# Optimization experiments

Measured on AMD Instinct MI355X. Metric: run time of the kernel, lower is better.

Reference implementation:

```python
import jax, jax.numpy as jnp
import numpy as np

D_MODEL = 1024
D_HEAD = 128
B, S = 4, 4096


def apply_rope(x, cos, sin):
    # x: [B,S,d_head], cos/sin: [S, d_head//2]
    half = x.shape[-1] // 2
    x1, x2 = x[..., :half], x[..., half:]
    cos = cos[None, :, :].astype(x.dtype)
    sin = sin[None, :, :].astype(x.dtype)
    return jnp.concatenate([x1 * cos - x2 * sin, x1 * sin + x2 * cos], axis=-1)


def setup_inputs() -> dict:
    key = jax.random.key(0)
    ks = jax.random.split(key, 10)
    x = jax.random.normal(ks[0], (B, S, D_MODEL), dtype=jnp.float32)
    # realistic RoPE tables
    half = D_HEAD // 2
    inv_freq = 1.0 / (10000.0 ** (np.arange(0, half, dtype=np.float32) / half))
    pos = np.arange(S, dtype=np.float32)
    ang = pos[:, None] * inv_freq[None, :]
    cos = jnp.asarray(np.cos(ang), dtype=jnp.float32)
    sin = jnp.asarray(np.sin(ang), dtype=jnp.float32)
    # True where key index > query index (masked positions)
    causal_mask = jnp.triu(jnp.ones((S, S), dtype=bool), k=1)
    scale_w = 1.0 / np.sqrt(D_MODEL)
    Wq1 = jax.random.normal(ks[1], (D_MODEL, D_HEAD), dtype=jnp.float32) * scale_w
    Wq2 = jax.random.normal(ks[2], (D_MODEL, D_HEAD), dtype=jnp.float32) * scale_w
    Wk1 = jax.random.normal(ks[3], (D_MODEL, D_HEAD), dtype=jnp.float32) * scale_w
    Wk2 = jax.random.normal(ks[4], (D_MODEL, D_HEAD), dtype=jnp.float32) * scale_w
    Wv = jax.random.normal(ks[5], (D_MODEL, D_HEAD), dtype=jnp.float32) * scale_w
    Wo = jax.random.normal(ks[6], (D_HEAD, D_MODEL), dtype=jnp.float32) * (1.0 / np.sqrt(D_HEAD))
    return {"x": x, "cos": cos, "sin": sin, "causal_mask": causal_mask,
            "Wq1": Wq1, "Wq2": Wq2, "Wk1": Wk1, "Wk2": Wk2, "Wv": Wv, "Wo": Wo}


def reference(x, cos, sin, causal_mask, Wq1, Wq2, Wk1, Wk2, Wv, Wo):
    q1 = apply_rope(jnp.einsum('bsD,Dd->bsd', x, Wq1), cos, sin)
    q2 = apply_rope(jnp.einsum('bsD,Dd->bsd', x, Wq2), cos, sin)
    k1 = apply_rope(jnp.einsum('bsD,Dd->bsd', x, Wk1), cos, sin)
    k2 = apply_rope(jnp.einsum('bsD,Dd->bsd', x, Wk2), cos, sin)
    v = jnp.einsum('bsD,Dd->bsd', x, Wv)
    scale = 1.0 / np.sqrt(D_HEAD)
    a1 = jnp.einsum('bsd,btd->bst', q1, k1) * scale
    a2 = jnp.einsum('bsd,btd->bst', q2, k2) * scale
    a = jnp.where(causal_mask[None, :, :], 0.0, a1 * a2)
    out = jnp.einsum('bst,btd->bsd', a, v)
    return jnp.einsum('bsd,dD->bsD', out, Wo)
```

## Files before the change

kernel.cpp:

```cpp
#include <hip/hip_runtime.h>
#include <stdint.h>
#include <stddef.h>

typedef _Float16 f16;
typedef __attribute__((ext_vector_type(8))) _Float16 f16x8;
typedef __attribute__((ext_vector_type(4))) _Float16 f16x4;
typedef __attribute__((ext_vector_type(16))) float f32x16;
typedef __attribute__((ext_vector_type(4))) float floatx4;

#define MFMA(a, b, c) __builtin_amdgcn_mfma_f32_32x32x16_f16((a), (b), (c), 0, 0, 0)

typedef const __attribute__((address_space(1))) void gvoid_t;
typedef __attribute__((address_space(3))) void svoid_t;

__device__ __forceinline__ void gload_lds16(const void* g, void* l) {
  __builtin_amdgcn_global_load_lds((gvoid_t*)g, (svoid_t*)l, 16, 0, 0);
}

__global__ __launch_bounds__(256) void k_cvt_f16(const float* __restrict__ in,
                                                 f16* __restrict__ out, int n4) {
  int i = blockIdx.x * 256 + threadIdx.x;
  if (i < n4) {
    floatx4 v = ((const floatx4*)in)[i];
    f16x4 o;
    o[0] = (f16)v[0]; o[1] = (f16)v[1]; o[2] = (f16)v[2]; o[3] = (f16)v[3];
    ((f16x4*)out)[i] = o;
  }
}

__global__ __launch_bounds__(256) void k_transpose_cvt(const float* __restrict__ W,
                                                       f16* __restrict__ Wt, int K, int N) {
  __shared__ float t[32][33];
  int k0 = blockIdx.x * 32, n0 = blockIdx.y * 32;
  int tx = threadIdx.x & 31, ty = threadIdx.x >> 5;
#pragma unroll
  for (int i = 0; i < 4; ++i)
    t[ty + 8 * i][tx] = W[(size_t)(k0 + ty + 8 * i) * N + n0 + tx];
  __syncthreads();
#pragma unroll
  for (int i = 0; i < 4; ++i)
    Wt[(size_t)(n0 + ty + 8 * i) * K + k0 + tx] = (f16)t[tx][ty + 8 * i];
}

__global__ __launch_bounds__(256, 2) void k_gemm(const f16* __restrict__ A,
                                                 const f16* __restrict__ Bt,
                                                 float* __restrict__ C,
                                                 int M, int N, int K) {
  __shared__ __align__(16) f16 As[128 * 64];
  __shared__ __align__(16) f16 Bs[128 * 64];
  int tid = threadIdx.x;
  int wave = tid >> 6, lane = tid & 63;
  int m0 = blockIdx.y * 128, n0 = blockIdx.x * 128;
  int wm = (wave >> 1) * 64, wn = (wave & 1) * 64;
  int rl = lane & 31, h = lane >> 5;
  int srow = lane >> 3, sslot = lane & 7;

  f32x16 acc[2][2];
#pragma unroll
  for (int mb = 0; mb < 2; ++mb)
#pragma unroll
    for (int nb = 0; nb < 2; ++nb)
#pragma unroll
      for (int r = 0; r < 16; ++r) acc[mb][nb][r] = 0.f;

  for (int k0 = 0; k0 < K; k0 += 64) {
    __syncthreads();
#pragma unroll
    for (int c = 0; c < 4; ++c) {
      int chunk = c * 4 + wave;
      int r = chunk * 8 + srow;
      int cb = sslot ^ (r & 7);
      gload_lds16(A + (size_t)(m0 + r) * K + k0 + cb * 8, As + chunk * 512);
      gload_lds16(Bt + (size_t)(n0 + r) * K + k0 + cb * 8, Bs + chunk * 512);
    }
    __syncthreads();

#pragma unroll
    for (int kb = 0; kb < 4; ++kb) {
      int s = 2 * kb + h;
      f16x8 af[2], bf[2];
#pragma unroll
      for (int mb = 0; mb < 2; ++mb) {
        int r = wm + mb * 32 + rl;
        af[mb] = *(const f16x8*)(As + r * 64 + (s ^ (r & 7)) * 8);
      }
#pragma unroll
      for (int nb = 0; nb < 2; ++nb) {
        int r = wn + nb * 32 + rl;
        bf[nb] = *(const f16x8*)(Bs + r * 64 + (s ^ (r & 7)) * 8);
      }
#pragma unroll
      for (int mb = 0; mb < 2; ++mb)
#pragma unroll
        for (int nb = 0; nb < 2; ++nb)
          acc[mb][nb] = MFMA(af[mb], bf[nb], acc[mb][nb]);
    }
  }

#pragma unroll
  for (int mb = 0; mb < 2; ++mb)
#pragma unroll
    for (int nb = 0; nb < 2; ++nb)
#pragma unroll
      for (int r = 0; r < 16; ++r) {
        int i = m0 + wm + mb * 32 + (r & 3) + 8 * (r >> 2) + 4 * h;
        int j = n0 + wn + nb * 32 + rl;
        C[(size_t)i * N + j] = acc[mb][nb][r];
      }
}

__global__ __launch_bounds__(256, 2) void k_proj(const f16* __restrict__ A,
                                                 const f16* __restrict__ Bt,
                                                 const float* __restrict__ cosp,
                                                 const float* __restrict__ sinp,
                                                 f16* __restrict__ q1h, f16* __restrict__ q2h,
                                                 f16* __restrict__ k1h, f16* __restrict__ k2h,
                                                 f16* __restrict__ vh) {
  __shared__ __align__(16) f16 As[128 * 64];
  __shared__ __align__(16) f16 Bs[128 * 64];
  int tid = threadIdx.x;
  int wave = tid >> 6, lane = tid & 63;
  int m0 = blockIdx.y * 128, n0 = blockIdx.x;
  int wm = wave * 32;
  int rl = lane & 31, h = lane >> 5;
  int srow = lane >> 3, sslot = lane & 7;
  const f16* Bmat = Bt + (size_t)n0 * 128 * 1024;

  f32x16 acc[4];
#pragma unroll
  for (int nb = 0; nb < 4; ++nb)
#pragma unroll
    for (int r = 0; r < 16; ++r) acc[nb][r] = 0.f;

  for (int k0 = 0; k0 < 1024; k0 += 64) {
    __syncthreads();
#pragma unroll
    for (int c = 0; c < 4; ++c) {
      int chunk = c * 4 + wave;
      int r = chunk * 8 + srow;
      int cb = sslot ^ (r & 7);
      gload_lds16(A + (size_t)(m0 + r) * 1024 + k0 + cb * 8, As + chunk * 512);
      gload_lds16(Bmat + (size_t)r * 1024 + k0 + cb * 8, Bs + chunk * 512);
    }
    __syncthreads();

#pragma unroll
    for (int kb = 0; kb < 4; ++kb) {
      int s = 2 * kb + h;
      int ra = wm + rl;
      f16x8 af = *(const f16x8*)(As + ra * 64 + (s ^ (ra & 7)) * 8);
      f16x8 bf[4];
#pragma unroll
      for (int nb = 0; nb < 4; ++nb) {
        int rb = nb * 32 + rl;
        bf[nb] = *(const f16x8*)(Bs + rb * 64 + (s ^ (rb & 7)) * 8);
      }
#pragma unroll
      for (int nb = 0; nb < 4; ++nb) acc[nb] = MFMA(af, bf[nb], acc[nb]);
    }
  }

  if (n0 == 4) {
#pragma unroll
    for (int r = 0; r < 16; ++r) {
      int irow = (r & 3) + 8 * (r >> 2) + 4 * h;
      int gr = m0 + wm + irow;
#pragma unroll
      for (int nb = 0; nb < 4; ++nb)
        vh[(size_t)gr * 128 + nb * 32 + rl] = (f16)acc[nb][r];
    }
  } else {
    f16* outp = (n0 == 0) ? q1h : (n0 == 1) ? q2h : (n0 == 2) ? k1h : k2h;
#pragma unroll
    for (int r = 0; r < 16; ++r) {
      int irow = (r & 3) + 8 * (r >> 2) + 4 * h;
      int gr = m0 + wm + irow;
      int s = gr & 4095;
#pragma unroll
      for (int nb = 0; nb < 2; ++nb) {
        int d = nb * 32 + rl;
        float c = cosp[s * 64 + d], sn = sinp[s * 64 + d];
        float a = acc[nb][r], bb = acc[nb + 2][r];
        outp[(size_t)gr * 128 + d]      = (f16)(a * c - bb * sn);
        outp[(size_t)gr * 128 + 64 + d] = (f16)(a * sn + bb * c);
      }
    }
  }
}

__global__ __launch_bounds__(256) void k_vtrans16(const f16* __restrict__ vh,
                                                  f16* __restrict__ vt) {
  __shared__ unsigned short t[32][33];
  int r0 = blockIdx.x * 32, d0 = blockIdx.y * 32;
  int tx = threadIdx.x & 31, ty = threadIdx.x >> 5;
#pragma unroll
  for (int i = 0; i < 4; ++i)
    t[ty + 8 * i][tx] = ((const unsigned short*)vh)[(size_t)(r0 + ty + 8 * i) * 128 + d0 + tx];
  __syncthreads();
  int b = r0 >> 12, s0 = r0 & 4095;
#pragma unroll
  for (int i = 0; i < 4; ++i)
    ((unsigned short*)vt)[((size_t)(b * 128 + d0 + ty + 8 * i)) * 4096 + s0 + tx] =
        t[tx][ty + 8 * i];
}

__global__ __launch_bounds__(256, 2) void k_s(const f16* __restrict__ q1h,
                                              const f16* __restrict__ q2h,
                                              const f16* __restrict__ k1h,
                                              const f16* __restrict__ k2h,
                                              f16* __restrict__ P) {
  __shared__ __align__(16) f16 A1[128 * 64];
  __shared__ __align__(16) f16 A2[128 * 64];
  __shared__ __align__(16) f16 B1[128 * 64];
  __shared__ __align__(16) f16 B2[128 * 64];
  int bid0 = blockIdx.x;
  int bid = (bid0 & 7) * 264 + (bid0 >> 3);
  int b = bid / 528, t = bid % 528;
  int i = (int)((sqrtf(8.f * t + 1.f) - 1.f) * 0.5f);
  if ((i + 1) * (i + 2) / 2 <= t) ++i;
  if (i * (i + 1) / 2 > t) --i;
  int j = t - i * (i + 1) / 2;

  int tid = threadIdx.x;
  int wave = tid >> 6, lane = tid & 63;
  int wm = (wave >> 1) * 64, wn = (wave & 1) * 64;
  int rl = lane & 31, h = lane >> 5;
  int srow = lane >> 3, sslot = lane & 7;
  size_t rowA = (size_t)b * 4096 + i * 128;
  size_t rowB = (size_t)b * 4096 + j * 128;

  f32x16 acc1[2][2], acc2[2][2];
#pragma unroll
  for (int mb = 0; mb < 2; ++mb)
#pragma unroll
    for (int nb = 0; nb < 2; ++nb)
#pragma unroll
      for (int r = 0; r < 16; ++r) { acc1[mb][nb][r] = 0.f; acc2[mb][nb][r] = 0.f; }

  for (int k0 = 0; k0 < 128; k0 += 64) {
    __syncthreads();
#pragma unroll
    for (int c = 0; c < 4; ++c) {
      int chunk = c * 4 + wave;
      int r = chunk * 8 + srow;
      int cb = sslot ^ (r & 7);
      gload_lds16(q1h + (rowA + r) * 128 + k0 + cb * 8, A1 + chunk * 512);
      gload_lds16(q2h + (rowA + r) * 128 + k0 + cb * 8, A2 + chunk * 512);
      gload_lds16(k1h + (rowB + r) * 128 + k0 + cb * 8, B1 + chunk * 512);
      gload_lds16(k2h + (rowB + r) * 128 + k0 + cb * 8, B2 + chunk * 512);
    }
    __syncthreads();

#pragma unroll
    for (int kb = 0; kb < 4; ++kb) {
      int s = 2 * kb + h;
      f16x8 a1f[2], a2f[2], b1f[2], b2f[2];
#pragma unroll
      for (int mb = 0; mb < 2; ++mb) {
        int r = wm + mb * 32 + rl;
        int off = r * 64 + (s ^ (r & 7)) * 8;
        a1f[mb] = *(const f16x8*)(A1 + off);
        a2f[mb] = *(const f16x8*)(A2 + off);
      }
#pragma unroll
      for (int nb = 0; nb < 2; ++nb) {
        int r = wn + nb * 32 + rl;
        int off = r * 64 + (s ^ (r & 7)) * 8;
        b1f[nb] = *(const f16x8*)(B1 + off);
        b2f[nb] = *(const f16x8*)(B2 + off);
      }
#pragma unroll
      for (int mb = 0; mb < 2; ++mb)
#pragma unroll
        for (int nb = 0; nb < 2; ++nb) {
          acc1[mb][nb] = MFMA(a1f[mb], b1f[nb], acc1[mb][nb]);
          acc2[mb][nb] = MFMA(a2f[mb], b2f[nb], acc2[mb][nb]);
        }
    }
  }

  f16* pt = P + ((size_t)b * 528 + t) * 16384;
  bool diag = (i == j);
#pragma unroll
  for (int mb = 0; mb < 2; ++mb)
#pragma unroll
    for (int nb = 0; nb < 2; ++nb)
#pragma unroll
      for (int r = 0; r < 16; ++r) {
        int row_l = wm + mb * 32 + (r & 3) + 8 * (r >> 2) + 4 * h;
        int col_l = wn + nb * 32 + rl;
        float p = acc1[mb][nb][r] * acc2[mb][nb][r] * (1.0f / 128.0f);
        if (diag && col_l > row_l) p = 0.f;
        pt[(size_t)row_l * 128 + col_l] = (f16)p;
      }
}

__global__ __launch_bounds__(256, 2) void k_pv(const f16* __restrict__ P,
                                               const f16* __restrict__ vt,
                                               float* __restrict__ o0, float* __restrict__ o1,
                                               float* __restrict__ o2, float* __restrict__ o3) {
  __shared__ __align__(16) f16 As[128 * 64];
  __shared__ __align__(16) f16 Bs[128 * 64];
  int bid = blockIdx.x;
  int b = bid / 80, c = bid % 80;
  int qt, s;
  if (c < 8)       { qt = c;                 s = 0; }
  else if (c < 24) { int t = c - 8;  qt = 8  + (t >> 1); s = t & 1; }
  else if (c < 48) { int t = c - 24; qt = 16 + t / 3;    s = t - 3 * (t / 3); }
  else             { int t = c - 48; qt = 24 + (t >> 2); s = t & 3; }
  int tq = qt * (qt + 1) / 2;
  const f16* Pb = P + (size_t)b * 528 * 16384;
  const f16* vb = vt + (size_t)b * 128 * 4096;
  int kbase = s * 1024;
  int kend = (qt + 1) * 128 < kbase + 1024 ? (qt + 1) * 128 : kbase + 1024;

  int tid = threadIdx.x;
  int wave = tid >> 6, lane = tid & 63;
  int wm = (wave >> 1) * 64, wn = (wave & 1) * 64;
  int rl = lane & 31, h = lane >> 5;
  int srow = lane >> 3, sslot = lane & 7;

  f32x16 acc[2][2];
#pragma unroll
  for (int mb = 0; mb < 2; ++mb)
#pragma unroll
    for (int nb = 0; nb < 2; ++nb)
#pragma unroll
      for (int r = 0; r < 16; ++r) acc[mb][nb][r] = 0.f;

  for (int k0 = kbase; k0 < kend; k0 += 64) {
    int jt = k0 >> 7, koff = k0 & 127;
    const f16* Pt = Pb + (size_t)(tq + jt) * 16384;
    __syncthreads();
#pragma unroll
    for (int c4 = 0; c4 < 4; ++c4) {
      int chunk = c4 * 4 + wave;
      int r = chunk * 8 + srow;
      int cb = sslot ^ (r & 7);
      gload_lds16(Pt + (size_t)r * 128 + koff + cb * 8, As + chunk * 512);
      gload_lds16(vb + (size_t)r * 4096 + k0 + cb * 8, Bs + chunk * 512);
    }
    __syncthreads();

#pragma unroll
    for (int kb = 0; kb < 4; ++kb) {
      int sidx = 2 * kb + h;
      f16x8 af[2], bf[2];
#pragma unroll
      for (int mb = 0; mb < 2; ++mb) {
        int r = wm + mb * 32 + rl;
        af[mb] = *(const f16x8*)(As + r * 64 + (sidx ^ (r & 7)) * 8);
      }
#pragma unroll
      for (int nb = 0; nb < 2; ++nb) {
        int r = wn + nb * 32 + rl;
        bf[nb] = *(const f16x8*)(Bs + r * 64 + (sidx ^ (r & 7)) * 8);
      }
#pragma unroll
      for (int mb = 0; mb < 2; ++mb)
#pragma unroll
        for (int nb = 0; nb < 2; ++nb)
          acc[mb][nb] = MFMA(af[mb], bf[nb], acc[mb][nb]);
    }
  }

  float* op = (s == 0) ? o0 : (s == 1) ? o1 : (s == 2) ? o2 : o3;
#pragma unroll
  for (int mb = 0; mb < 2; ++mb)
#pragma unroll
    for (int nb = 0; nb < 2; ++nb)
#pragma unroll
      for (int r = 0; r < 16; ++r) {
        int gr = b * 4096 + qt * 128 + wm + mb * 32 + (r & 3) + 8 * (r >> 2) + 4 * h;
        op[(size_t)gr * 128 + wn + nb * 32 + rl] = acc[mb][nb][r];
      }
}

__global__ __launch_bounds__(256) void k_comb(const float* __restrict__ o0,
                                              const float* __restrict__ o1,
                                              const float* __restrict__ o2,
                                              const float* __restrict__ o3,
                                              f16* __restrict__ oh) {
  int idx = blockIdx.x * 256 + threadIdx.x;
  int row = idx >> 5;
  int qt = (row & 4095) >> 7;
  int ns = (qt >> 3) + 1;
  floatx4 v = ((const floatx4*)o0)[idx];
  if (ns > 1) { floatx4 w = ((const floatx4*)o1)[idx]; v[0]+=w[0]; v[1]+=w[1]; v[2]+=w[2]; v[3]+=w[3]; }
  if (ns > 2) { floatx4 w = ((const floatx4*)o2)[idx]; v[0]+=w[0]; v[1]+=w[1]; v[2]+=w[2]; v[3]+=w[3]; }
  if (ns > 3) { floatx4 w = ((const floatx4*)o3)[idx]; v[0]+=w[0]; v[1]+=w[1]; v[2]+=w[2]; v[3]+=w[3]; }
  f16x4 r4;
#pragma unroll
  for (int k = 0; k < 4; ++k) r4[k] = (f16)v[k];
  ((f16x4*)oh)[idx] = r4;
}

extern "C" void kernel_launch(void* const* d_in, const int* in_sizes, int n_in,
                              void* d_out, int out_size, void* d_ws, size_t ws_size,
                              hipStream_t stream) {
  (void)in_sizes; (void)n_in; (void)out_size; (void)ws_size;
  const float* x  = (const float*)d_in[0];
  const float* cp = (const float*)d_in[1];
  const float* sp = (const float*)d_in[2];
  const float* W[5] = {(const float*)d_in[4], (const float*)d_in[5], (const float*)d_in[6],
                       (const float*)d_in[7], (const float*)d_in[8]};
  const float* Wo = (const float*)d_in[9];
  float* out = (float*)d_out;
  char* ws = (char*)d_ws;

  const size_t OFF_H    = 33554432;
  const size_t OFF_WTH  = OFF_H + 7 * 4194304;
  const size_t OFF_WOTH = OFF_WTH + 1310720;
  const size_t OFF_P    = OFF_WOTH + 262144;
  f16*   xh   = (f16*)(ws + 0);
  float* o0   = (float*)(ws + 0);
  float* o1   = (float*)(ws + 8388608);
  float* o2   = (float*)(ws + 16777216);
  float* o3   = (float*)(ws + 25165824);
  f16*   q1h  = (f16*)(ws + OFF_H + 0 * 4194304);
  f16*   q2h  = (f16*)(ws + OFF_H + 1 * 4194304);
  f16*   k1h  = (f16*)(ws + OFF_H + 2 * 4194304);
  f16*   k2h  = (f16*)(ws + OFF_H + 3 * 4194304);
  f16*   vh   = (f16*)(ws + OFF_H + 4 * 4194304);
  f16*   vt   = (f16*)(ws + OFF_H + 5 * 4194304);
  f16*   oh   = (f16*)(ws + OFF_H + 6 * 4194304);
  f16*   Wth  = (f16*)(ws + OFF_WTH);
  f16*   Woth = (f16*)(ws + OFF_WOTH);
  f16*   P    = (f16*)(ws + OFF_P);

  k_cvt_f16<<<16384, 256, 0, stream>>>(x, xh, 4194304);
  for (int w = 0; w < 5; ++w)
    k_transpose_cvt<<<dim3(32, 4), 256, 0, stream>>>(W[w], Wth + (size_t)w * 128 * 1024, 1024, 128);
  k_transpose_cvt<<<dim3(4, 32), 256, 0, stream>>>(Wo, Woth, 128, 1024);
  k_proj<<<dim3(5, 128), 256, 0, stream>>>(xh, Wth, cp, sp, q1h, q2h, k1h, k2h, vh);
  k_vtrans16<<<dim3(512, 4), 256, 0, stream>>>(vh, vt);
  k_s<<<2112, 256, 0, stream>>>(q1h, q2h, k1h, k2h, P);
  k_pv<<<320, 256, 0, stream>>>(P, vt, o0, o1, o2, o3);
  k_comb<<<2048, 256, 0, stream>>>(o0, o1, o2, o3, oh);
  k_gemm<<<dim3(8, 128), 256, 0, stream>>>(oh, Woth, out, 16384, 1024, 128);
}
```

Measured before the change: 150.6 us.

## Fuse x fp16 conversion into projection and split-combine into output GEMM

The projection kernel now loads fp32 x straight into LDS and converts to fp16 when reading fragments, which removes the separate conversion kernel and its round trip through memory. The PV partial outputs are stored as fp16 instead of fp32, and the output GEMM sums the split partials while staging its A tile, which removes the combine kernel. In exchange the projection's A tile doubles in LDS size (which may hurt occupancy), each partial is rounded to fp16 before summation, and the combine reads are repeated across the 8 N-tiles of the output GEMM.

```diff
diff --git a/kernel.cpp b/kernel.cpp
--- a/kernel.cpp
+++ b/kernel.cpp
@@ -6,6 +6,7 @@
 typedef __attribute__((ext_vector_type(8))) _Float16 f16x8;
 typedef __attribute__((ext_vector_type(4))) _Float16 f16x4;
 typedef __attribute__((ext_vector_type(16))) float f32x16;
+typedef __attribute__((ext_vector_type(8))) float f32x8v;
 typedef __attribute__((ext_vector_type(4))) float floatx4;
 
 #define MFMA(a, b, c) __builtin_amdgcn_mfma_f32_32x32x16_f16((a), (b), (c), 0, 0, 0)
@@ -15,17 +16,6 @@
 
 __device__ __forceinline__ void gload_lds16(const void* g, void* l) {
   __builtin_amdgcn_global_load_lds((gvoid_t*)g, (svoid_t*)l, 16, 0, 0);
-}
-
-__global__ __launch_bounds__(256) void k_cvt_f16(const float* __restrict__ in,
-                                                 f16* __restrict__ out, int n4) {
-  int i = blockIdx.x * 256 + threadIdx.x;
-  if (i < n4) {
-    floatx4 v = ((const floatx4*)in)[i];
-    f16x4 o;
-    o[0] = (f16)v[0]; o[1] = (f16)v[1]; o[2] = (f16)v[2]; o[3] = (f16)v[3];
-    ((f16x4*)out)[i] = o;
-  }
 }
 
 __global__ __launch_bounds__(256) void k_transpose_cvt(const float* __restrict__ W,
@@ -42,81 +32,14 @@
     Wt[(size_t)(n0 + ty + 8 * i) * K + k0 + tx] = (f16)t[tx][ty + 8 * i];
 }
 
-__global__ __launch_bounds__(256, 2) void k_gemm(const f16* __restrict__ A,
-                                                 const f16* __restrict__ Bt,
-                                                 float* __restrict__ C,
-                                                 int M, int N, int K) {
-  __shared__ __align__(16) f16 As[128 * 64];
-  __shared__ __align__(16) f16 Bs[128 * 64];
-  int tid = threadIdx.x;
-  int wave = tid >> 6, lane = tid & 63;
-  int m0 = blockIdx.y * 128, n0 = blockIdx.x * 128;
-  int wm = (wave >> 1) * 64, wn = (wave & 1) * 64;
-  int rl = lane & 31, h = lane >> 5;
-  int srow = lane >> 3, sslot = lane & 7;
-
-  f32x16 acc[2][2];
-#pragma unroll
-  for (int mb = 0; mb < 2; ++mb)
-#pragma unroll
-    for (int nb = 0; nb < 2; ++nb)
-#pragma unroll
-      for (int r = 0; r < 16; ++r) acc[mb][nb][r] = 0.f;
-
-  for (int k0 = 0; k0 < K; k0 += 64) {
-    __syncthreads();
-#pragma unroll
-    for (int c = 0; c < 4; ++c) {
-      int chunk = c * 4 + wave;
-      int r = chunk * 8 + srow;
-      int cb = sslot ^ (r & 7);
-      gload_lds16(A + (size_t)(m0 + r) * K + k0 + cb * 8, As + chunk * 512);
-      gload_lds16(Bt + (size_t)(n0 + r) * K + k0 + cb * 8, Bs + chunk * 512);
-    }
-    __syncthreads();
-
-#pragma unroll
-    for (int kb = 0; kb < 4; ++kb) {
-      int s = 2 * kb + h;
-      f16x8 af[2], bf[2];
-#pragma unroll
-      for (int mb = 0; mb < 2; ++mb) {
-        int r = wm + mb * 32 + rl;
-        af[mb] = *(const f16x8*)(As + r * 64 + (s ^ (r & 7)) * 8);
-      }
-#pragma unroll
-      for (int nb = 0; nb < 2; ++nb) {
-        int r = wn + nb * 32 + rl;
-        bf[nb] = *(const f16x8*)(Bs + r * 64 + (s ^ (r & 7)) * 8);
-      }
-#pragma unroll
-      for (int mb = 0; mb < 2; ++mb)
-#pragma unroll
-        for (int nb = 0; nb < 2; ++nb)
-          acc[mb][nb] = MFMA(af[mb], bf[nb], acc[mb][nb]);
-    }
-  }
-
-#pragma unroll
-  for (int mb = 0; mb < 2; ++mb)
-#pragma unroll
-    for (int nb = 0; nb < 2; ++nb)
-#pragma unroll
-      for (int r = 0; r < 16; ++r) {
-        int i = m0 + wm + mb * 32 + (r & 3) + 8 * (r >> 2) + 4 * h;
-        int j = n0 + wn + nb * 32 + rl;
-        C[(size_t)i * N + j] = acc[mb][nb][r];
-      }
-}
-
-__global__ __launch_bounds__(256, 2) void k_proj(const f16* __restrict__ A,
+__global__ __launch_bounds__(256, 2) void k_proj(const float* __restrict__ X,
                                                  const f16* __restrict__ Bt,
                                                  const float* __restrict__ cosp,
                                                  const float* __restrict__ sinp,
                                                  f16* __restrict__ q1h, f16* __restrict__ q2h,
                                                  f16* __restrict__ k1h, f16* __restrict__ k2h,
                                                  f16* __restrict__ vh) {
-  __shared__ __align__(16) f16 As[128 * 64];
+  __shared__ __align__(16) float Af[128 * 64];
   __shared__ __align__(16) f16 Bs[128 * 64];
   int tid = threadIdx.x;
   int wave = tid >> 6, lane = tid & 63;
@@ -124,6 +47,7 @@
   int wm = wave * 32;
   int rl = lane & 31, h = lane >> 5;
   int srow = lane >> 3, sslot = lane & 7;
+  int arow = lane >> 4, aslot = lane & 15;
   const f16* Bmat = Bt + (size_t)n0 * 128 * 1024;
 
   f32x16 acc[4];
@@ -134,12 +58,18 @@
 
   for (int k0 = 0; k0 < 1024; k0 += 64) {
     __syncthreads();
+#pragma unroll
+    for (int c = 0; c < 8; ++c) {
+      int chunk = c * 4 + wave;
+      int r = chunk * 4 + arow;
+      int src16 = (((aslot >> 1) ^ (r & 7)) << 1) | (aslot & 1);
+      gload_lds16(X + (size_t)(m0 + r) * 1024 + k0 + src16 * 4, Af + chunk * 256);
+    }
 #pragma unroll
     for (int c = 0; c < 4; ++c) {
       int chunk = c * 4 + wave;
       int r = chunk * 8 + srow;
       int cb = sslot ^ (r & 7);
-      gload_lds16(A + (size_t)(m0 + r) * 1024 + k0 + cb * 8, As + chunk * 512);
       gload_lds16(Bmat + (size_t)r * 1024 + k0 + cb * 8, Bs + chunk * 512);
     }
     __syncthreads();
@@ -148,7 +78,10 @@
     for (int kb = 0; kb < 4; ++kb) {
       int s = 2 * kb + h;
       int ra = wm + rl;
-      f16x8 af = *(const f16x8*)(As + ra * 64 + (s ^ (ra & 7)) * 8);
+      f32x8v a8 = *(const f32x8v*)(Af + ra * 64 + ((s ^ (ra & 7)) * 8));
+      f16x8 af;
+#pragma unroll
+      for (int e = 0; e < 8; ++e) af[e] = (f16)a8[e];
       f16x8 bf[4];
 #pragma unroll
       for (int nb = 0; nb < 4; ++nb) {
@@ -297,8 +230,8 @@
 
 __global__ __launch_bounds__(256, 2) void k_pv(const f16* __restrict__ P,
                                                const f16* __restrict__ vt,
-                                               float* __restrict__ o0, float* __restrict__ o1,
-                                               float* __restrict__ o2, float* __restrict__ o3) {
+                                               f16* __restrict__ o0, f16* __restrict__ o1,
+                                               f16* __restrict__ o2, f16* __restrict__ o3) {
   __shared__ __align__(16) f16 As[128 * 64];
   __shared__ __align__(16) f16 Bs[128 * 64];
   int bid = blockIdx.x;
@@ -364,7 +297,7 @@
     }
   }
 
-  float* op = (s == 0) ? o0 : (s == 1) ? o1 : (s == 2) ? o2 : o3;
+  f16* op = (s == 0) ? o0 : (s == 1) ? o1 : (s == 2) ? o2 : o3;
 #pragma unroll
   for (int mb = 0; mb < 2; ++mb)
 #pragma unroll
@@ -372,27 +305,94 @@
 #pragma unroll
       for (int r = 0; r < 16; ++r) {
         int gr = b * 4096 + qt * 128 + wm + mb * 32 + (r & 3) + 8 * (r >> 2) + 4 * h;
-        op[(size_t)gr * 128 + wn + nb * 32 + rl] = acc[mb][nb][r];
-      }
-}
-
-__global__ __launch_bounds__(256) void k_comb(const float* __restrict__ o0,
-                                              const float* __restrict__ o1,
-                                              const float* __restrict__ o2,
-                                              const float* __restrict__ o3,
-                                              f16* __restrict__ oh) {
-  int idx = blockIdx.x * 256 + threadIdx.x;
-  int row = idx >> 5;
-  int qt = (row & 4095) >> 7;
+        op[(size_t)gr * 128 + wn + nb * 32 + rl] = (f16)acc[mb][nb][r];
+      }
+}
+
+__global__ __launch_bounds__(256, 2) void k_gout(const f16* __restrict__ o0,
+                                                 const f16* __restrict__ o1,
+                                                 const f16* __restrict__ o2,
+                                                 const f16* __restrict__ o3,
+                                                 const f16* __restrict__ Bt,
+                                                 float* __restrict__ C) {
+  __shared__ __align__(16) f16 As[128 * 64];
+  __shared__ __align__(16) f16 Bs[128 * 64];
+  int tid = threadIdx.x;
+  int wave = tid >> 6, lane = tid & 63;
+  int m0 = blockIdx.y * 128, n0 = blockIdx.x * 128;
+  int wm = (wave >> 1) * 64, wn = (wave & 1) * 64;
+  int rl = lane & 31, h = lane >> 5;
+  int srow = lane >> 3, sslot = lane & 7;
+  int qt = (m0 >> 7) & 31;
   int ns = (qt >> 3) + 1;
-  floatx4 v = ((const floatx4*)o0)[idx];
-  if (ns > 1) { floatx4 w = ((const floatx4*)o1)[idx]; v[0]+=w[0]; v[1]+=w[1]; v[2]+=w[2]; v[3]+=w[3]; }
-  if (ns > 2) { floatx4 w = ((const floatx4*)o2)[idx]; v[0]+=w[0]; v[1]+=w[1]; v[2]+=w[2]; v[3]+=w[3]; }
-  if (ns > 3) { floatx4 w = ((const floatx4*)o3)[idx]; v[0]+=w[0]; v[1]+=w[1]; v[2]+=w[2]; v[3]+=w[3]; }
-  f16x4 r4;
-#pragma unroll
-  for (int k = 0; k < 4; ++k) r4[k] = (f16)v[k];
-  ((f16x4*)oh)[idx] = r4;
+  const f16* srcs[4] = {o0, o1, o2, o3};
+
+  f32x16 acc[2][2];
+#pragma unroll
+  for (int mb = 0; mb < 2; ++mb)
+#pragma unroll
+    for (int nb = 0; nb < 2; ++nb)
+#pragma unroll
+      for (int r = 0; r < 16; ++r) acc[mb][nb][r] = 0.f;
+
+  for (int k0 = 0; k0 < 128; k0 += 64) {
+    __syncthreads();
+#pragma unroll
+    for (int c = 0; c < 4; ++c) {
+      int chunk = c * 4 + wave;
+      int r = chunk * 8 + srow;
+      float sum[8];
+#pragma unroll
+      for (int e = 0; e < 8; ++e) sum[e] = 0.f;
+#pragma unroll
+      for (int p = 0; p < 4; ++p) {
+        if (p < ns) {
+          f16x8 v = *(const f16x8*)(srcs[p] + (size_t)(m0 + r) * 128 + k0 + sslot * 8);
+#pragma unroll
+          for (int e = 0; e < 8; ++e) sum[e] += (float)v[e];
+        }
+      }
+      f16x8 w;
+#pragma unroll
+      for (int e = 0; e < 8; ++e) w[e] = (f16)sum[e];
+      *(f16x8*)(As + r * 64 + (sslot ^ (r & 7)) * 8) = w;
+      int cb = sslot ^ (r & 7);
+      gload_lds16(Bt + (size_t)(n0 + r) * 128 + k0 + cb * 8, Bs + chunk * 512);
+    }
+    __syncthreads();
+
+#pragma unroll
+    for (int kb = 0; kb < 4; ++kb) {
+      int s = 2 * kb + h;
+      f16x8 af[2], bf[2];
+#pragma unroll
+      for (int mb = 0; mb < 2; ++mb) {
+        int r = wm + mb * 32 + rl;
+        af[mb] = *(const f16x8*)(As + r * 64 + (s ^ (r & 7)) * 8);
+      }
+#pragma unroll
+      for (int nb = 0; nb < 2; ++nb) {
+        int r = wn + nb * 32 + rl;
+        bf[nb] = *(const f16x8*)(Bs + r * 64 + (s ^ (r & 7)) * 8);
+      }
+#pragma unroll
+      for (int mb = 0; mb < 2; ++mb)
+#pragma unroll
+        for (int nb = 0; nb < 2; ++nb)
+          acc[mb][nb] = MFMA(af[mb], bf[nb], acc[mb][nb]);
+    }
+  }
+
+#pragma unroll
+  for (int mb = 0; mb < 2; ++mb)
+#pragma unroll
+    for (int nb = 0; nb < 2; ++nb)
+#pragma unroll
+      for (int r = 0; r < 16; ++r) {
+        int i = m0 + wm + mb * 32 + (r & 3) + 8 * (r >> 2) + 4 * h;
+        int j = n0 + wn + nb * 32 + rl;
+        C[(size_t)i * 1024 + j] = acc[mb][nb][r];
+      }
 }
 
 extern "C" void kernel_launch(void* const* d_in, const int* in_sizes, int n_in,
@@ -409,33 +409,29 @@
   char* ws = (char*)d_ws;
 
   const size_t OFF_H    = 33554432;
-  const size_t OFF_WTH  = OFF_H + 7 * 4194304;
+  const size_t OFF_WTH  = OFF_H + 6 * 4194304;
   const size_t OFF_WOTH = OFF_WTH + 1310720;
   const size_t OFF_P    = OFF_WOTH + 262144;
-  f16*   xh   = (f16*)(ws + 0);
-  float* o0   = (float*)(ws + 0);
-  float* o1   = (float*)(ws + 8388608);
-  float* o2   = (float*)(ws + 16777216);
-  float* o3   = (float*)(ws + 25165824);
+  f16*   o0   = (f16*)(ws + 0);
+  f16*   o1   = (f16*)(ws + 4194304);
+  f16*   o2   = (f16*)(ws + 8388608);
+  f16*   o3   = (f16*)(ws + 12582912);
   f16*   q1h  = (f16*)(ws + OFF_H + 0 * 4194304);
   f16*   q2h  = (f16*)(ws + OFF_H + 1 * 4194304);
   f16*   k1h  = (f16*)(ws + OFF_H + 2 * 4194304);
   f16*   k2h  = (f16*)(ws + OFF_H + 3 * 4194304);
   f16*   vh   = (f16*)(ws + OFF_H + 4 * 4194304);
   f16*   vt   = (f16*)(ws + OFF_H + 5 * 4194304);
-  f16*   oh   = (f16*)(ws + OFF_H + 6 * 4194304);
   f16*   Wth  = (f16*)(ws + OFF_WTH);
   f16*   Woth = (f16*)(ws + OFF_WOTH);
   f16*   P    = (f16*)(ws + OFF_P);
 
-  k_cvt_f16<<<16384, 256, 0, stream>>>(x, xh, 4194304);
   for (int w = 0; w < 5; ++w)
     k_transpose_cvt<<<dim3(32, 4), 256, 0, stream>>>(W[w], Wth + (size_t)w * 128 * 1024, 1024, 128);
   k_transpose_cvt<<<dim3(4, 32), 256, 0, stream>>>(Wo, Woth, 128, 1024);
-  k_proj<<<dim3(5, 128), 256, 0, stream>>>(xh, Wth, cp, sp, q1h, q2h, k1h, k2h, vh);
+  k_proj<<<dim3(5, 128), 256, 0, stream>>>(x, Wth, cp, sp, q1h, q2h, k1h, k2h, vh);
   k_vtrans16<<<dim3(512, 4), 256, 0, stream>>>(vh, vt);
   k_s<<<2112, 256, 0, stream>>>(q1h, q2h, k1h, k2h, P);
   k_pv<<<320, 256, 0, stream>>>(P, vt, o0, o1, o2, o3);
-  k_comb<<<2048, 256, 0, stream>>>(o0, o1, o2, o3, oh);
-  k_gemm<<<dim3(8, 128), 256, 0, stream>>>(oh, Woth, out, 16384, 1024, 128);
-}
+  k_gout<<<dim3(8, 128), 256, 0, stream>>>(o0, o1, o2, o3, Woth, out);
+}
```

Result: slower. 163.5 us (+8.6%).
